# Optimization experiments

Hardware: AMD Instinct MI355X
Metric: run time of the kernel (lower is better)

## Reference

```python
import jax, jax.numpy as jnp
import numpy as np

U, IS, IT, D, DEG, L = 50000, 25000, 25000, 128, 16, 3


def _bipartite(key, n_users, n_items, deg):
    # symmetric normalized bipartite adjacency in COO, nnz = 2*n_users*deg
    ki = jax.random.fold_in(key, 1)
    u = jnp.repeat(jnp.arange(n_users, dtype=jnp.int32), deg)
    it = jax.random.randint(ki, (n_users * deg,), 0, n_items, dtype=jnp.int32)
    rows = jnp.concatenate([u, n_users + it])
    cols = jnp.concatenate([n_users + it, u])
    vals = jnp.full(rows.shape, 1.0 / deg, dtype=jnp.float32)
    return rows, cols, vals


def setup_inputs() -> dict:
    key = jax.random.key(0)
    ks = jax.random.split(key, 16)
    sc = 0.1
    inp = {
        'emb_s_user': jax.random.normal(ks[0], (U, D), jnp.float32) * sc,
        'emb_s_item': jax.random.normal(ks[1], (IS, D), jnp.float32) * sc,
        'emb_t_user': jax.random.normal(ks[2], (U, D), jnp.float32) * sc,
        'emb_t_item': jax.random.normal(ks[3], (IT, D), jnp.float32) * sc,
        'emb_share_user': jax.random.normal(ks[4], (U, D), jnp.float32) * sc,
    }
    inp['s_rows'], inp['s_cols'], inp['s_vals'] = _bipartite(ks[5], U, IS, DEG)
    inp['t_rows'], inp['t_cols'], inp['t_vals'] = _bipartite(ks[6], U, IT, DEG)
    inp['c_rows'], inp['c_cols'], inp['c_vals'] = _bipartite(ks[7], U, IS + IT, 2 * DEG)
    def lin(k, fi, fo):
        b = float(np.sqrt(6.0 / (fi + fo)))
        return jax.random.uniform(k, (fi, fo), jnp.float32, -b, b)
    inp.update({
        'Wd1': lin(ks[8], D, D), 'bd1': jnp.zeros((D,), jnp.float32),
        'Wd2': lin(ks[9], D, 2 * D), 'bd2': jnp.zeros((2 * D,), jnp.float32),
        'Wa1_s': lin(ks[10], 3 * D, D), 'ba1_s': jnp.zeros((D,), jnp.float32),
        'Wa2_s': lin(ks[11], D, 3), 'ba2_s': jnp.zeros((3,), jnp.float32),
        'Wa1_t': lin(ks[12], 3 * D, D), 'ba1_t': jnp.zeros((D,), jnp.float32),
        'Wa2_t': lin(ks[13], D, 3), 'ba2_t': jnp.zeros((3,), jnp.float32),
    })
    return inp


def _spmm(rows, cols, vals, x, n):
    # y = A @ x, A sparse COO (n x n)
    return jax.ops.segment_sum(vals[:, None] * x[cols], rows, num_segments=n)


def _lightgcn(rows, cols, vals, emb, n):
    acc, h = emb, emb
    for _ in range(L):  # layer-accumulating SpMM (mean of layer outputs)
        h = _spmm(rows, cols, vals, h, n)
        acc = acc + h
    return acc / (L + 1)


def _fuse(spe, intm, pop, W1, b1, W2, b2):
    x = jnp.concatenate([spe, intm, pop], axis=1)          # [B, 3D]
    h = jax.nn.relu(x @ W1 + b1)                           # [B, D]
    w = jax.nn.softmax(h @ W2 + b2, axis=1)                # [B, 3]
    return spe * w[:, 0:1] + intm * w[:, 1:2] + pop * w[:, 2:3]


def reference(emb_s_user, emb_s_item, emb_t_user, emb_t_item, emb_share_user,
              s_rows, s_cols, s_vals, t_rows, t_cols, t_vals,
              c_rows, c_cols, c_vals,
              Wd1, bd1, Wd2, bd2,
              Wa1_s, ba1_s, Wa2_s, ba2_s, Wa1_t, ba1_t, Wa2_t, ba2_t):
    # LightGCN propagation over the three graphs (get_G_emb)
    es = _lightgcn(s_rows, s_cols, s_vals, jnp.concatenate([emb_s_user, emb_s_item], 0), U + IS)
    et = _lightgcn(t_rows, t_cols, t_vals, jnp.concatenate([emb_t_user, emb_t_item], 0), U + IT)
    ec = _lightgcn(c_rows, c_cols, c_vals,
                   jnp.concatenate([emb_share_user, emb_s_item, emb_t_item], 0), U + IS + IT)
    user_s, user_t, user_sha = es[:U], et[:U], ec[:U]
    # disen_encoder (dropout inactive in eval): int / pop split
    h = jax.nn.relu(user_sha @ Wd1 + bd1)
    ip = h @ Wd2 + bd2
    int_u, pop_u = ip[:, :D], ip[:, D:]
    fused_s = _fuse(user_s, int_u, pop_u, Wa1_s, ba1_s, Wa2_s, ba2_s)
    fused_t = _fuse(user_t, int_u, pop_u, Wa1_t, ba1_t, Wa2_t, ba2_t)
    return jnp.concatenate([fused_s, fused_t], axis=0)  # [2U, D]
```

## Files before the change

### kernel.cpp

```cpp
#include <hip/hip_runtime.h>
#include <math.h>

#define UN 50000
#define DD 128
#define NUTILE 3125

typedef __attribute__((ext_vector_type(4))) float f32x4;
typedef __attribute__((ext_vector_type(8))) short s16x8;
typedef __attribute__((ext_vector_type(8))) unsigned short u16x8;
typedef __attribute__((ext_vector_type(4))) _Float16 f16x4;
typedef __attribute__((ext_vector_type(8))) _Float16 f16x8;
typedef unsigned short ushort_t;

__device__ __forceinline__ f32x4 mfma16(s16x8 a, s16x8 b, f32x4 c) {
  return __builtin_amdgcn_mfma_f32_16x16x32_bf16(a, b, c, 0, 0, 0);
}

__device__ __forceinline__ void split8(const float* x, s16x8& hi, s16x8& lo) {
  #pragma unroll
  for (int i = 0; i < 8; ++i) {
    float xv = x[i];
    unsigned xb = __float_as_uint(xv);
    unsigned h16 = (xb + 0x7fffu + ((xb >> 16) & 1u)) >> 16;
    float hf = __uint_as_float(h16 << 16);
    float lf = xv - hf;
    unsigned lb = __float_as_uint(lf);
    unsigned l16 = (lb + 0x7fffu + ((lb >> 16) & 1u)) >> 16;
    hi[i] = (short)h16;
    lo[i] = (short)l16;
  }
}

__global__ void zero_ints_k(int* p, int n) {
  int i = blockIdx.x * 256 + threadIdx.x;
  if (i < n) p[i] = 0;
}

__global__ void count_items_k(const int* __restrict__ cols, int E2, int* __restrict__ counts) {
  int base = (blockIdx.x * 256 + threadIdx.x) * 4;
  if (base + 3 < E2) {
    int4 c = *(const int4*)(cols + base);
    atomicAdd(&counts[c.x - UN], 1);
    atomicAdd(&counts[c.y - UN], 1);
    atomicAdd(&counts[c.z - UN], 1);
    atomicAdd(&counts[c.w - UN], 1);
  } else {
    for (int k = 0; k < 4; ++k)
      if (base + k < E2) atomicAdd(&counts[cols[base + k] - UN], 1);
  }
}

__global__ void scanA_k(const int* __restrict__ counts, int n, int* __restrict__ bsum) {
  __shared__ int sd[256];
  int t = threadIdx.x;
  int base = blockIdx.x * 1024 + t * 4;
  int s = 0;
  if (base + 3 < n) {
    int4 v = *(const int4*)(counts + base);
    s = v.x + v.y + v.z + v.w;
  } else {
    for (int k = 0; k < 4; ++k) if (base + k < n) s += counts[base + k];
  }
  sd[t] = s;
  __syncthreads();
  for (int off = 128; off > 0; off >>= 1) {
    if (t < off) sd[t] += sd[t + off];
    __syncthreads();
  }
  if (t == 0) bsum[blockIdx.x] = sd[0];
}

__global__ void scanB_k(int* __restrict__ bsum, int G) {
  __shared__ int sd[64];
  int t = threadIdx.x;
  sd[t] = (t < G) ? bsum[t] : 0;
  __syncthreads();
  int acc = 0;
  for (int i = 0; i < t; ++i) acc += sd[i];
  if (t < G) bsum[t] = acc;
}

__global__ void scanC_k(int* __restrict__ counts, int* __restrict__ offsets, int n,
                        const int* __restrict__ bsum) {
  __shared__ int sd[256];
  int t = threadIdx.x;
  int base = blockIdx.x * 1024 + t * 4;
  int c[4];
  int s = 0;
  #pragma unroll
  for (int k = 0; k < 4; ++k) {
    int idx = base + k;
    c[k] = (idx < n) ? counts[idx] : 0;
    s += c[k];
  }
  sd[t] = s;
  __syncthreads();
  for (int off = 1; off < 256; off <<= 1) {
    int v = (t >= off) ? sd[t - off] : 0;
    __syncthreads();
    sd[t] += v;
    __syncthreads();
  }
  int run = bsum[blockIdx.x] + ((t == 0) ? 0 : sd[t - 1]);
  #pragma unroll
  for (int k = 0; k < 4; ++k) {
    int idx = base + k;
    if (idx < n) { offsets[idx] = run; run += c[k]; counts[idx] = 0; }
  }
  if (base <= n - 1 && n - 1 < base + 4) offsets[n] = run;
}

__global__ void fill_lists_k(const int* __restrict__ cols, int E2,
                             const int* __restrict__ offsets, int* __restrict__ cursor,
                             int* __restrict__ lists, int shift) {
  int base = (blockIdx.x * 256 + threadIdx.x) * 4;
  if (base + 3 < E2) {
    int4 c = *(const int4*)(cols + base);
    int it0 = c.x - UN, it1 = c.y - UN, it2 = c.z - UN, it3 = c.w - UN;
    lists[offsets[it0] + atomicAdd(&cursor[it0], 1)] = base >> shift;
    lists[offsets[it1] + atomicAdd(&cursor[it1], 1)] = (base + 1) >> shift;
    lists[offsets[it2] + atomicAdd(&cursor[it2], 1)] = (base + 2) >> shift;
    lists[offsets[it3] + atomicAdd(&cursor[it3], 1)] = (base + 3) >> shift;
  } else {
    for (int k = 0; k < 4; ++k) {
      if (base + k < E2) {
        int it = cols[base + k] - UN;
        lists[offsets[it] + atomicAdd(&cursor[it], 1)] = (base + k) >> shift;
      }
    }
  }
}

__global__ void conv16_k(const float* __restrict__ in, _Float16* __restrict__ out) {
  int i = blockIdx.x * 256 + threadIdx.x;
  f32x4 v = ((const f32x4*)in)[i];
  f16x4 o;
  o[0] = (_Float16)v[0]; o[1] = (_Float16)v[1]; o[2] = (_Float16)v[2]; o[3] = (_Float16)v[3];
  ((f16x4*)out)[i] = o;
}

__global__ void initconv_k(const float* __restrict__ emb, float* __restrict__ acc,
                           _Float16* __restrict__ ue) {
  int i = blockIdx.x * 256 + threadIdx.x;
  f32x4 v = ((const f32x4*)emb)[i];
  ((f32x4*)acc)[i] = v * 0.25f;
  f16x4 o;
  o[0] = (_Float16)v[0]; o[1] = (_Float16)v[1]; o[2] = (_Float16)v[2]; o[3] = (_Float16)v[3];
  ((f16x4*)ue)[i] = o;
}

template<int DEG, bool WRITE_U, bool HAS_ITEM>
__global__ void hop_k(const int* __restrict__ cols, const int* __restrict__ ioff,
                      const int* __restrict__ ilst, const float* __restrict__ vals,
                      const _Float16* __restrict__ isrc, const _Float16* __restrict__ usrc,
                      _Float16* __restrict__ uout, _Float16* __restrict__ iout,
                      float* __restrict__ acc, int nitems) {
  int wid = (blockIdx.x * blockDim.x + threadIdx.x) >> 6;
  int lane = threadIdx.x & 63;
  int q = lane >> 4, cl = lane & 15;
  float v = vals[0];
  float s[8] = {};
  if (wid < UN) {
    int ebase = wid * DEG;
    #pragma unroll
    for (int p = 0; p < DEG / 4; ++p) {
      int item = cols[ebase + 4 * p + q] - UN;
      f16x8 x = *(const f16x8*)(isrc + (size_t)item * DD + cl * 8);
      #pragma unroll
      for (int r = 0; r < 8; ++r) s[r] += (float)x[r];
    }
    #pragma unroll
    for (int r = 0; r < 8; ++r) {
      s[r] += __shfl_xor(s[r], 16, 64);
      s[r] += __shfl_xor(s[r], 32, 64);
      s[r] *= v;
    }
    if (lane < 16) {
      if (WRITE_U) {
        f16x8 o;
        #pragma unroll
        for (int r = 0; r < 8; ++r) o[r] = (_Float16)s[r];
        *(f16x8*)(uout + (size_t)wid * DD + cl * 8) = o;
      }
      float* ap = acc + (size_t)wid * DD + cl * 8;
      f32x4 a0 = *(f32x4*)ap;
      f32x4 a1 = *(f32x4*)(ap + 4);
      #pragma unroll
      for (int r = 0; r < 4; ++r) { a0[r] += 0.25f * s[r]; a1[r] += 0.25f * s[r + 4]; }
      *(f32x4*)ap = a0;
      *(f32x4*)(ap + 4) = a1;
    }
  } else if (HAS_ITEM) {
    int it = wid - UN;
    if (it >= nitems) return;
    int b = ioff[it], e = ioff[it + 1];
    for (int j = b + q; j < e; j += 4) {
      int u = ilst[j];
      f16x8 x = *(const f16x8*)(usrc + (size_t)u * DD + cl * 8);
      #pragma unroll
      for (int r = 0; r < 8; ++r) s[r] += (float)x[r];
    }
    #pragma unroll
    for (int r = 0; r < 8; ++r) {
      s[r] += __shfl_xor(s[r], 16, 64);
      s[r] += __shfl_xor(s[r], 32, 64);
    }
    if (lane < 16) {
      f16x8 o;
      #pragma unroll
      for (int r = 0; r < 8; ++r) o[r] = (_Float16)(v * s[r]);
      *(f16x8*)(iout + (size_t)it * DD + cl * 8) = o;
    }
  }
}

__global__ void wprep_k(const float* __restrict__ W, ushort_t* __restrict__ whi,
                        ushort_t* __restrict__ wlo, int K, int N) {
  int idx = blockIdx.x * 256 + threadIdx.x;
  if (idx >= K * N) return;
  int i = idx & 7, l = (idx >> 3) & 63, tt = idx >> 9;
  int NT = N >> 4;
  int t = tt % NT, c = tt / NT;
  int k = c * 32 + 8 * (l >> 4) + i;
  int n = t * 16 + (l & 15);
  float xv = W[k * N + n];
  unsigned xb = __float_as_uint(xv);
  unsigned h16 = (xb + 0x7fffu + ((xb >> 16) & 1u)) >> 16;
  float hf = __uint_as_float(h16 << 16);
  float lf = xv - hf;
  unsigned lb = __float_as_uint(lf);
  unsigned l16 = (lb + 0x7fffu + ((lb >> 16) & 1u)) >> 16;
  whi[idx] = (ushort_t)h16;
  wlo[idx] = (ushort_t)l16;
}

template<int NCH, int NT, bool RELU, bool OUT16>
__global__ __launch_bounds__(256) void gemm_mfma_k(const float* __restrict__ X,
    const ushort_t* __restrict__ whi, const ushort_t* __restrict__ wlo,
    const float* __restrict__ bias, void* __restrict__ Ov) {
  __shared__ ushort_t sh[NT * 512];
  __shared__ ushort_t sl[NT * 512];
  int tid = threadIdx.x, lane = tid & 63;
  int utile = blockIdx.x * 4 + (tid >> 6);
  bool act = utile < NUTILE;
  const float* xrow = X + (size_t)(utile * 16 + (lane & 15)) * (NCH * 32);
  f32x4 acc[NT] = {};
  for (int c = 0; c < NCH; ++c) {
    __syncthreads();
    for (int q = tid; q < NT * 64; q += 256) {
      ((u16x8*)sh)[q] = ((const u16x8*)(whi + c * NT * 512))[q];
      ((u16x8*)sl)[q] = ((const u16x8*)(wlo + c * NT * 512))[q];
    }
    __syncthreads();
    if (!act) continue;
    int k0 = c * 32 + 8 * (lane >> 4);
    f32x4 xa = *(const f32x4*)(xrow + k0);
    f32x4 xb = *(const f32x4*)(xrow + k0 + 4);
    float xs8[8] = {xa[0], xa[1], xa[2], xa[3], xb[0], xb[1], xb[2], xb[3]};
    s16x8 ahi, alo;
    split8(xs8, ahi, alo);
    #pragma unroll
    for (int t = 0; t < NT; ++t) {
      s16x8 bh = ((const s16x8*)sh)[t * 64 + lane];
      s16x8 bl = ((const s16x8*)sl)[t * 64 + lane];
      acc[t] = mfma16(ahi, bh, acc[t]);
      acc[t] = mfma16(alo, bh, acc[t]);
      acc[t] = mfma16(ahi, bl, acc[t]);
    }
  }
  if (!act) return;
  int g4 = 4 * (lane >> 4);
  #pragma unroll
  for (int t = 0; t < NT; ++t) {
    int col = t * 16 + (lane & 15);
    float bb = bias[col];
    #pragma unroll
    for (int r = 0; r < 4; ++r) {
      float vv = acc[t][r] + bb;
      if (RELU) vv = fmaxf(vv, 0.f);
      size_t oidx = (size_t)(utile * 16 + g4 + r) * (NT * 16) + col;
      if (OUT16) ((_Float16*)Ov)[oidx] = (_Float16)vv;
      else ((float*)Ov)[oidx] = vv;
    }
  }
}

__global__ __launch_bounds__(256) void fuse_mfma_k(
    const float* __restrict__ spe, const _Float16* __restrict__ ip,
    const ushort_t* __restrict__ whi, const ushort_t* __restrict__ wlo,
    const float* __restrict__ b1, const float* __restrict__ W2,
    const float* __restrict__ b2, float* __restrict__ outp) {
  __shared__ ushort_t sh[8 * 512];
  __shared__ ushort_t sl[8 * 512];
  int tid = threadIdx.x, lane = tid & 63;
  int utile = blockIdx.x * 4 + (tid >> 6);
  bool act = utile < NUTILE;
  int rowA = utile * 16 + (lane & 15);
  f32x4 acc[8] = {};
  for (int c = 0; c < 12; ++c) {
    __syncthreads();
    for (int q = tid; q < 512; q += 256) {
      ((u16x8*)sh)[q] = ((const u16x8*)(whi + c * 4096))[q];
      ((u16x8*)sl)[q] = ((const u16x8*)(wlo + c * 4096))[q];
    }
    __syncthreads();
    if (!act) continue;
    int k0 = c * 32 + 8 * (lane >> 4);
    float xs8[8];
    if (k0 < 128) {
      f32x4 xa = *(const f32x4*)(spe + (size_t)rowA * 128 + k0);
      f32x4 xb = *(const f32x4*)(spe + (size_t)rowA * 128 + k0 + 4);
      xs8[0] = xa[0]; xs8[1] = xa[1]; xs8[2] = xa[2]; xs8[3] = xa[3];
      xs8[4] = xb[0]; xs8[5] = xb[1]; xs8[6] = xb[2]; xs8[7] = xb[3];
    } else {
      f16x8 xh = *(const f16x8*)(ip + (size_t)rowA * 256 + (k0 - 128));
      #pragma unroll
      for (int r = 0; r < 8; ++r) xs8[r] = (float)xh[r];
    }
    s16x8 ahi, alo;
    split8(xs8, ahi, alo);
    #pragma unroll
    for (int t = 0; t < 8; ++t) {
      s16x8 bh = ((const s16x8*)sh)[t * 64 + lane];
      s16x8 bl = ((const s16x8*)sl)[t * 64 + lane];
      acc[t] = mfma16(ahi, bh, acc[t]);
      acc[t] = mfma16(alo, bh, acc[t]);
      acc[t] = mfma16(ahi, bl, acc[t]);
    }
  }
  if (!act) return;
  float lg0[4] = {}, lg1[4] = {}, lg2[4] = {};
  #pragma unroll
  for (int t = 0; t < 8; ++t) {
    int col = t * 16 + (lane & 15);
    float bb = b1[col];
    float w20 = W2[col * 3 + 0], w21 = W2[col * 3 + 1], w22 = W2[col * 3 + 2];
    #pragma unroll
    for (int r = 0; r < 4; ++r) {
      float hv = fmaxf(acc[t][r] + bb, 0.f);
      lg0[r] += hv * w20; lg1[r] += hv * w21; lg2[r] += hv * w22;
    }
  }
  #pragma unroll
  for (int off = 1; off < 16; off <<= 1) {
    #pragma unroll
    for (int r = 0; r < 4; ++r) {
      lg0[r] += __shfl_xor(lg0[r], off, 64);
      lg1[r] += __shfl_xor(lg1[r], off, 64);
      lg2[r] += __shfl_xor(lg2[r], off, 64);
    }
  }
  float b20 = b2[0], b21 = b2[1], b22 = b2[2];
  int g4 = 4 * (lane >> 4);
  #pragma unroll
  for (int r = 0; r < 4; ++r) {
    float l0 = lg0[r] + b20, l1 = lg1[r] + b21, l2 = lg2[r] + b22;
    float m = fmaxf(l0, fmaxf(l1, l2));
    float e0 = expf(l0 - m), e1 = expf(l1 - m), e2 = expf(l2 - m);
    float inv = 1.f / (e0 + e1 + e2);
    float w0 = e0 * inv, w1 = e1 * inv, w2 = e2 * inv;
    size_t row = (size_t)(utile * 16 + g4 + r);
    #pragma unroll
    for (int t = 0; t < 8; ++t) {
      int col = t * 16 + (lane & 15);
      float sp = spe[row * 128 + col];
      float iu = (float)ip[row * 256 + col];
      float pu = (float)ip[row * 256 + 128 + col];
      outp[row * 128 + col] = sp * w0 + iu * w1 + pu * w2;
    }
  }
}

extern "C" void kernel_launch(void* const* d_in, const int* in_sizes, int n_in,
                              void* d_out, int out_size, void* d_ws, size_t ws_size,
                              hipStream_t stream) {
  const float* emb_s_user = (const float*)d_in[0];
  const float* emb_s_item = (const float*)d_in[1];
  const float* emb_t_user = (const float*)d_in[2];
  const float* emb_t_item = (const float*)d_in[3];
  const float* emb_sh_user = (const float*)d_in[4];
  const int* s_cols = (const int*)d_in[6];
  const float* s_vals = (const float*)d_in[7];
  const int* t_cols = (const int*)d_in[9];
  const float* t_vals = (const float*)d_in[10];
  const int* c_cols = (const int*)d_in[12];
  const float* c_vals = (const float*)d_in[13];
  const float* Wd1 = (const float*)d_in[14];
  const float* bd1 = (const float*)d_in[15];
  const float* Wd2 = (const float*)d_in[16];
  const float* bd2 = (const float*)d_in[17];
  const float* Wa1_s = (const float*)d_in[18];
  const float* ba1_s = (const float*)d_in[19];
  const float* Wa2_s = (const float*)d_in[20];
  const float* ba2_s = (const float*)d_in[21];
  const float* Wa1_t = (const float*)d_in[22];
  const float* ba1_t = (const float*)d_in[23];
  const float* Wa2_t = (const float*)d_in[24];
  const float* ba2_t = (const float*)d_in[25];

  char* wsb = (char*)d_ws;
  float* acc = (float*)wsb;
  _Float16* ip16 = (_Float16*)(wsb + 25600000);
  _Float16* u1 = (_Float16*)(wsb + 51200000);
  _Float16* i1 = (_Float16*)(wsb + 64000000);
  float* H = (float*)(wsb + 51200000);
  _Float16* i2 = (_Float16*)(wsb + 76800000);
  _Float16* ue = i2;
  _Float16* ie = (_Float16*)(wsb + 89600000);
  ushort_t* wbase = (ushort_t*)(wsb + 102400000);
  ushort_t* wd1h = wbase;
  ushort_t* wd1l = wbase + 16384;
  ushort_t* wd2h = wbase + 32768;
  ushort_t* wd2l = wbase + 65536;
  ushort_t* wa1sh = wbase + 98304;
  ushort_t* wa1sl = wbase + 147456;
  ushort_t* wa1th = wbase + 196608;
  ushort_t* wa1tl = wbase + 245760;
  int* ioff = (int*)(wsb + 103040000);
  int* icnt = (int*)(wsb + 103260032);
  int* bsum = (int*)(wsb + 103460096);
  int* ilst = (int*)(wsb + 103460608);

  float* outp = (float*)d_out;

  wprep_k<<<64, 256, 0, stream>>>(Wd1, wd1h, wd1l, 128, 128);
  wprep_k<<<128, 256, 0, stream>>>(Wd2, wd2h, wd2l, 128, 256);
  wprep_k<<<192, 256, 0, stream>>>(Wa1_s, wa1sh, wa1sl, 384, 128);
  wprep_k<<<192, 256, 0, stream>>>(Wa1_t, wa1th, wa1tl, 384, 128);
  conv16_k<<<3125, 256, 0, stream>>>(emb_s_item, ie);
  conv16_k<<<3125, 256, 0, stream>>>(emb_t_item, ie + (size_t)25000 * DD);

  auto run_graph = [&](const int* cols, const float* vals, int deg, int shift, int nitems,
                       const float* embU, const _Float16* isrc) {
    int E2 = UN * deg;
    int gE4 = (E2 + 1023) / 1024;
    int G = (nitems + 1023) / 1024;
    zero_ints_k<<<(nitems + 255) / 256, 256, 0, stream>>>(icnt, nitems);
    count_items_k<<<gE4, 256, 0, stream>>>(cols, E2, icnt);
    scanA_k<<<G, 256, 0, stream>>>(icnt, nitems, bsum);
    scanB_k<<<1, 64, 0, stream>>>(bsum, G);
    scanC_k<<<G, 256, 0, stream>>>(icnt, ioff, nitems, bsum);
    fill_lists_k<<<gE4, 256, 0, stream>>>(cols, E2, ioff, icnt, ilst, shift);
    initconv_k<<<6250, 256, 0, stream>>>(embU, acc, ue);
    int gH = (UN + nitems) / 4;
    int gU = UN / 4;
    if (deg == 32) {
      hop_k<32, true, true><<<gH, 256, 0, stream>>>(cols, ioff, ilst, vals, isrc, ue, u1, i1, acc, nitems);
      hop_k<32, false, true><<<gH, 256, 0, stream>>>(cols, ioff, ilst, vals, i1, u1, nullptr, i2, acc, nitems);
      hop_k<32, false, false><<<gU, 256, 0, stream>>>(cols, ioff, ilst, vals, i2, nullptr, nullptr, nullptr, acc, nitems);
    } else {
      hop_k<16, true, true><<<gH, 256, 0, stream>>>(cols, ioff, ilst, vals, isrc, ue, u1, i1, acc, nitems);
      hop_k<16, false, true><<<gH, 256, 0, stream>>>(cols, ioff, ilst, vals, i1, u1, nullptr, i2, acc, nitems);
      hop_k<16, false, false><<<gU, 256, 0, stream>>>(cols, ioff, ilst, vals, i2, nullptr, nullptr, nullptr, acc, nitems);
    }
  };

  run_graph(c_cols, c_vals, 32, 5, 50000, emb_sh_user, ie);
  gemm_mfma_k<4, 8, true, false><<<782, 256, 0, stream>>>(acc, wd1h, wd1l, bd1, H);
  gemm_mfma_k<4, 16, false, true><<<782, 256, 0, stream>>>(H, wd2h, wd2l, bd2, ip16);
  run_graph(s_cols, s_vals, 16, 4, 25000, emb_s_user, ie);
  fuse_mfma_k<<<782, 256, 0, stream>>>(acc, ip16, wa1sh, wa1sl, ba1_s, Wa2_s, ba2_s, outp);
  run_graph(t_cols, t_vals, 16, 4, 25000, emb_t_user, ie + (size_t)25000 * DD);
  fuse_mfma_k<<<782, 256, 0, stream>>>(acc, ip16, wa1th, wa1tl, ba1_t, Wa2_t, ba2_t, outp + (size_t)UN * DD);

  (void)in_sizes; (void)n_in; (void)out_size; (void)ws_size;
}
```

Measured before the change: 1.211 ms.

## Batch CSR build across graphs, drop fp32 accumulator, store fp16 hop outputs

The transpose-list construction for all three graphs now runs once, batched through combined count, scan and fill kernels, and the item lists are stored as 16-bit indices. The per-hop read-modify-write of an fp32 accumulator is removed. Each hop instead writes its fp16 user output, and the final hop averages the embedding and the three layer outputs into one fp16 result. The GEMM and fuse kernels read that result as fp16. Weight prep is merged into a single launch and index loads use nontemporal hints. This cuts launch count and memory traffic, at the cost of extra fp16 rounding of the accumulated embeddings.

```diff
diff --git a/kernel.cpp b/kernel.cpp
--- a/kernel.cpp
+++ b/kernel.cpp
@@ -31,22 +31,41 @@
   }
 }
 
-__global__ void zero_ints_k(int* p, int n) {
+__global__ void zero_k(int* p, int n) {
   int i = blockIdx.x * 256 + threadIdx.x;
   if (i < n) p[i] = 0;
 }
 
-__global__ void count_items_k(const int* __restrict__ cols, int E2, int* __restrict__ counts) {
-  int base = (blockIdx.x * 256 + threadIdx.x) * 4;
-  if (base + 3 < E2) {
-    int4 c = *(const int4*)(cols + base);
-    atomicAdd(&counts[c.x - UN], 1);
-    atomicAdd(&counts[c.y - UN], 1);
-    atomicAdd(&counts[c.z - UN], 1);
-    atomicAdd(&counts[c.w - UN], 1);
+__global__ void conv16_k(const float* __restrict__ in, _Float16* __restrict__ out) {
+  int i = blockIdx.x * 256 + threadIdx.x;
+  f32x4 v = ((const f32x4*)in)[i];
+  f16x4 o;
+  o[0] = (_Float16)v[0]; o[1] = (_Float16)v[1]; o[2] = (_Float16)v[2]; o[3] = (_Float16)v[3];
+  ((f16x4*)out)[i] = o;
+}
+
+#define CBLK 1563
+#define SBLK 782
+#define EC 1600000
+#define ES 800000
+
+__global__ void count_all_k(const int* __restrict__ cc, const int* __restrict__ sc,
+                            const int* __restrict__ tc, int* __restrict__ counts) {
+  int b = blockIdx.x, t = threadIdx.x;
+  const int* cols; int E, base, b0;
+  if (b < CBLK) { cols = cc; E = EC; base = 0; b0 = 0; }
+  else if (b < CBLK + SBLK) { cols = sc; E = ES; base = 50000; b0 = CBLK; }
+  else { cols = tc; E = ES; base = 75000; b0 = CBLK + SBLK; }
+  int e = (b - b0) * 1024 + t * 4;
+  if (e + 3 < E) {
+    int4 c4 = *(const int4*)(cols + e);
+    atomicAdd(&counts[base + c4.x - UN], 1);
+    atomicAdd(&counts[base + c4.y - UN], 1);
+    atomicAdd(&counts[base + c4.z - UN], 1);
+    atomicAdd(&counts[base + c4.w - UN], 1);
   } else {
     for (int k = 0; k < 4; ++k)
-      if (base + k < E2) atomicAdd(&counts[cols[base + k] - UN], 1);
+      if (e + k < E) atomicAdd(&counts[base + cols[e + k] - UN], 1);
   }
 }
 
@@ -71,13 +90,13 @@
 }
 
 __global__ void scanB_k(int* __restrict__ bsum, int G) {
-  __shared__ int sd[64];
+  __shared__ int sd[128];
   int t = threadIdx.x;
   sd[t] = (t < G) ? bsum[t] : 0;
   __syncthreads();
-  int acc = 0;
-  for (int i = 0; i < t; ++i) acc += sd[i];
-  if (t < G) bsum[t] = acc;
+  int a = 0;
+  for (int i = 0; i < t; ++i) a += sd[i];
+  if (t < G) bsum[t] = a;
 }
 
 __global__ void scanC_k(int* __restrict__ counts, int* __restrict__ offsets, int n,
@@ -110,51 +129,40 @@
   if (base <= n - 1 && n - 1 < base + 4) offsets[n] = run;
 }
 
-__global__ void fill_lists_k(const int* __restrict__ cols, int E2,
-                             const int* __restrict__ offsets, int* __restrict__ cursor,
-                             int* __restrict__ lists, int shift) {
-  int base = (blockIdx.x * 256 + threadIdx.x) * 4;
-  if (base + 3 < E2) {
-    int4 c = *(const int4*)(cols + base);
-    int it0 = c.x - UN, it1 = c.y - UN, it2 = c.z - UN, it3 = c.w - UN;
-    lists[offsets[it0] + atomicAdd(&cursor[it0], 1)] = base >> shift;
-    lists[offsets[it1] + atomicAdd(&cursor[it1], 1)] = (base + 1) >> shift;
-    lists[offsets[it2] + atomicAdd(&cursor[it2], 1)] = (base + 2) >> shift;
-    lists[offsets[it3] + atomicAdd(&cursor[it3], 1)] = (base + 3) >> shift;
+__global__ void fill_all_k(const int* __restrict__ cc, const int* __restrict__ sc,
+                           const int* __restrict__ tc, const int* __restrict__ offsets,
+                           int* __restrict__ cursor, ushort_t* __restrict__ lists) {
+  int b = blockIdx.x, t = threadIdx.x;
+  const int* cols; int E, base, b0, shift;
+  if (b < CBLK) { cols = cc; E = EC; base = 0; b0 = 0; shift = 5; }
+  else if (b < CBLK + SBLK) { cols = sc; E = ES; base = 50000; b0 = CBLK; shift = 4; }
+  else { cols = tc; E = ES; base = 75000; b0 = CBLK + SBLK; shift = 4; }
+  int e = (b - b0) * 1024 + t * 4;
+  if (e + 3 < E) {
+    int4 c4 = *(const int4*)(cols + e);
+    int b0i = base + c4.x - UN, b1i = base + c4.y - UN, b2i = base + c4.z - UN, b3i = base + c4.w - UN;
+    lists[offsets[b0i] + atomicAdd(&cursor[b0i], 1)] = (ushort_t)(e >> shift);
+    lists[offsets[b1i] + atomicAdd(&cursor[b1i], 1)] = (ushort_t)((e + 1) >> shift);
+    lists[offsets[b2i] + atomicAdd(&cursor[b2i], 1)] = (ushort_t)((e + 2) >> shift);
+    lists[offsets[b3i] + atomicAdd(&cursor[b3i], 1)] = (ushort_t)((e + 3) >> shift);
   } else {
     for (int k = 0; k < 4; ++k) {
-      if (base + k < E2) {
-        int it = cols[base + k] - UN;
-        lists[offsets[it] + atomicAdd(&cursor[it], 1)] = (base + k) >> shift;
+      if (e + k < E) {
+        int bi = base + cols[e + k] - UN;
+        lists[offsets[bi] + atomicAdd(&cursor[bi], 1)] = (ushort_t)((e + k) >> shift);
       }
     }
   }
 }
 
-__global__ void conv16_k(const float* __restrict__ in, _Float16* __restrict__ out) {
-  int i = blockIdx.x * 256 + threadIdx.x;
-  f32x4 v = ((const f32x4*)in)[i];
-  f16x4 o;
-  o[0] = (_Float16)v[0]; o[1] = (_Float16)v[1]; o[2] = (_Float16)v[2]; o[3] = (_Float16)v[3];
-  ((f16x4*)out)[i] = o;
-}
-
-__global__ void initconv_k(const float* __restrict__ emb, float* __restrict__ acc,
-                           _Float16* __restrict__ ue) {
-  int i = blockIdx.x * 256 + threadIdx.x;
-  f32x4 v = ((const f32x4*)emb)[i];
-  ((f32x4*)acc)[i] = v * 0.25f;
-  f16x4 o;
-  o[0] = (_Float16)v[0]; o[1] = (_Float16)v[1]; o[2] = (_Float16)v[2]; o[3] = (_Float16)v[3];
-  ((f16x4*)ue)[i] = o;
-}
-
-template<int DEG, bool WRITE_U, bool HAS_ITEM>
-__global__ void hop_k(const int* __restrict__ cols, const int* __restrict__ ioff,
-                      const int* __restrict__ ilst, const float* __restrict__ vals,
-                      const _Float16* __restrict__ isrc, const _Float16* __restrict__ usrc,
-                      _Float16* __restrict__ uout, _Float16* __restrict__ iout,
-                      float* __restrict__ acc, int nitems) {
+template<int DEG, int PH>
+__global__ __launch_bounds__(256) void hop_k(
+    const int* __restrict__ cols, const int* __restrict__ ioffg,
+    const ushort_t* __restrict__ ilst, const float* __restrict__ vals,
+    const _Float16* __restrict__ gu, const _Float16* __restrict__ gi,
+    const _Float16* __restrict__ ue, const _Float16* __restrict__ u1,
+    const _Float16* __restrict__ u2,
+    _Float16* __restrict__ uout, _Float16* __restrict__ iout, int nitems) {
   int wid = (blockIdx.x * blockDim.x + threadIdx.x) >> 6;
   int lane = threadIdx.x & 63;
   int q = lane >> 4, cl = lane & 15;
@@ -164,8 +172,8 @@
     int ebase = wid * DEG;
     #pragma unroll
     for (int p = 0; p < DEG / 4; ++p) {
-      int item = cols[ebase + 4 * p + q] - UN;
-      f16x8 x = *(const f16x8*)(isrc + (size_t)item * DD + cl * 8);
+      int item = __builtin_nontemporal_load(&cols[ebase + 4 * p + q]) - UN;
+      f16x8 x = *(const f16x8*)(gu + (size_t)item * DD + cl * 8);
       #pragma unroll
       for (int r = 0; r < 8; ++r) s[r] += (float)x[r];
     }
@@ -176,27 +184,30 @@
       s[r] *= v;
     }
     if (lane < 16) {
-      if (WRITE_U) {
+      size_t ro = (size_t)wid * DD + cl * 8;
+      if (PH == 3) {
+        f16x8 a = *(const f16x8*)(ue + ro);
+        f16x8 b = *(const f16x8*)(u1 + ro);
+        f16x8 c2 = *(const f16x8*)(u2 + ro);
+        f16x8 o;
+        #pragma unroll
+        for (int r = 0; r < 8; ++r)
+          o[r] = (_Float16)(0.25f * ((float)a[r] + (float)b[r] + (float)c2[r] + s[r]));
+        *(f16x8*)(uout + ro) = o;
+      } else {
         f16x8 o;
         #pragma unroll
         for (int r = 0; r < 8; ++r) o[r] = (_Float16)s[r];
-        *(f16x8*)(uout + (size_t)wid * DD + cl * 8) = o;
+        *(f16x8*)(uout + ro) = o;
       }
-      float* ap = acc + (size_t)wid * DD + cl * 8;
-      f32x4 a0 = *(f32x4*)ap;
-      f32x4 a1 = *(f32x4*)(ap + 4);
-      #pragma unroll
-      for (int r = 0; r < 4; ++r) { a0[r] += 0.25f * s[r]; a1[r] += 0.25f * s[r + 4]; }
-      *(f32x4*)ap = a0;
-      *(f32x4*)(ap + 4) = a1;
-    }
-  } else if (HAS_ITEM) {
+    }
+  } else if (PH != 3) {
     int it = wid - UN;
     if (it >= nitems) return;
-    int b = ioff[it], e = ioff[it + 1];
+    int b = ioffg[it], e = ioffg[it + 1];
     for (int j = b + q; j < e; j += 4) {
-      int u = ilst[j];
-      f16x8 x = *(const f16x8*)(usrc + (size_t)u * DD + cl * 8);
+      int u = (int)__builtin_nontemporal_load(&ilst[j]);
+      f16x8 x = *(const f16x8*)(gi + (size_t)u * DD + cl * 8);
       #pragma unroll
       for (int r = 0; r < 8; ++r) s[r] += (float)x[r];
     }
@@ -214,10 +225,18 @@
   }
 }
 
-__global__ void wprep_k(const float* __restrict__ W, ushort_t* __restrict__ whi,
-                        ushort_t* __restrict__ wlo, int K, int N) {
-  int idx = blockIdx.x * 256 + threadIdx.x;
-  if (idx >= K * N) return;
+__global__ void wprep_all_k(const float* __restrict__ Wd1, const float* __restrict__ Wd2,
+                            const float* __restrict__ Wa1s, const float* __restrict__ Wa1t,
+                            ushort_t* __restrict__ wd1h, ushort_t* __restrict__ wd1l,
+                            ushort_t* __restrict__ wd2h, ushort_t* __restrict__ wd2l,
+                            ushort_t* __restrict__ wash, ushort_t* __restrict__ wasl,
+                            ushort_t* __restrict__ wath, ushort_t* __restrict__ watl) {
+  int b = blockIdx.x, tid = threadIdx.x;
+  const float* W; ushort_t *wh, *wl; int N, idx;
+  if (b < 64)       { W = Wd1;  wh = wd1h; wl = wd1l; N = 128; idx = b * 256 + tid; }
+  else if (b < 192) { W = Wd2;  wh = wd2h; wl = wd2l; N = 256; idx = (b - 64) * 256 + tid; }
+  else if (b < 384) { W = Wa1s; wh = wash; wl = wasl; N = 128; idx = (b - 192) * 256 + tid; }
+  else              { W = Wa1t; wh = wath; wl = watl; N = 128; idx = (b - 384) * 256 + tid; }
   int i = idx & 7, l = (idx >> 3) & 63, tt = idx >> 9;
   int NT = N >> 4;
   int t = tt % NT, c = tt / NT;
@@ -230,12 +249,12 @@
   float lf = xv - hf;
   unsigned lb = __float_as_uint(lf);
   unsigned l16 = (lb + 0x7fffu + ((lb >> 16) & 1u)) >> 16;
-  whi[idx] = (ushort_t)h16;
-  wlo[idx] = (ushort_t)l16;
-}
-
-template<int NCH, int NT, bool RELU, bool OUT16>
-__global__ __launch_bounds__(256) void gemm_mfma_k(const float* __restrict__ X,
+  wh[idx] = (ushort_t)h16;
+  wl[idx] = (ushort_t)l16;
+}
+
+template<int NCH, int NT, bool RELU, bool OUT16, bool XF16>
+__global__ __launch_bounds__(256) void gemm_mfma_k(const void* __restrict__ Xv,
     const ushort_t* __restrict__ whi, const ushort_t* __restrict__ wlo,
     const float* __restrict__ bias, void* __restrict__ Ov) {
   __shared__ ushort_t sh[NT * 512];
@@ -243,7 +262,7 @@
   int tid = threadIdx.x, lane = tid & 63;
   int utile = blockIdx.x * 4 + (tid >> 6);
   bool act = utile < NUTILE;
-  const float* xrow = X + (size_t)(utile * 16 + (lane & 15)) * (NCH * 32);
+  size_t rowA = (size_t)(utile * 16 + (lane & 15)) * (NCH * 32);
   f32x4 acc[NT] = {};
   for (int c = 0; c < NCH; ++c) {
     __syncthreads();
@@ -254,9 +273,17 @@
     __syncthreads();
     if (!act) continue;
     int k0 = c * 32 + 8 * (lane >> 4);
-    f32x4 xa = *(const f32x4*)(xrow + k0);
-    f32x4 xb = *(const f32x4*)(xrow + k0 + 4);
-    float xs8[8] = {xa[0], xa[1], xa[2], xa[3], xb[0], xb[1], xb[2], xb[3]};
+    float xs8[8];
+    if (XF16) {
+      f16x8 xh = *(const f16x8*)((const _Float16*)Xv + rowA + k0);
+      #pragma unroll
+      for (int r = 0; r < 8; ++r) xs8[r] = (float)xh[r];
+    } else {
+      f32x4 xa = *(const f32x4*)((const float*)Xv + rowA + k0);
+      f32x4 xb = *(const f32x4*)((const float*)Xv + rowA + k0 + 4);
+      xs8[0] = xa[0]; xs8[1] = xa[1]; xs8[2] = xa[2]; xs8[3] = xa[3];
+      xs8[4] = xb[0]; xs8[5] = xb[1]; xs8[6] = xb[2]; xs8[7] = xb[3];
+    }
     s16x8 ahi, alo;
     split8(xs8, ahi, alo);
     #pragma unroll
@@ -286,7 +313,7 @@
 }
 
 __global__ __launch_bounds__(256) void fuse_mfma_k(
-    const float* __restrict__ spe, const _Float16* __restrict__ ip,
+    const _Float16* __restrict__ spe, const _Float16* __restrict__ ip,
     const ushort_t* __restrict__ whi, const ushort_t* __restrict__ wlo,
     const float* __restrict__ b1, const float* __restrict__ W2,
     const float* __restrict__ b2, float* __restrict__ outp) {
@@ -306,17 +333,12 @@
     __syncthreads();
     if (!act) continue;
     int k0 = c * 32 + 8 * (lane >> 4);
+    f16x8 xh;
+    if (k0 < 128) xh = *(const f16x8*)(spe + (size_t)rowA * 128 + k0);
+    else xh = *(const f16x8*)(ip + (size_t)rowA * 256 + (k0 - 128));
     float xs8[8];
-    if (k0 < 128) {
-      f32x4 xa = *(const f32x4*)(spe + (size_t)rowA * 128 + k0);
-      f32x4 xb = *(const f32x4*)(spe + (size_t)rowA * 128 + k0 + 4);
-      xs8[0] = xa[0]; xs8[1] = xa[1]; xs8[2] = xa[2]; xs8[3] = xa[3];
-      xs8[4] = xb[0]; xs8[5] = xb[1]; xs8[6] = xb[2]; xs8[7] = xb[3];
-    } else {
-      f16x8 xh = *(const f16x8*)(ip + (size_t)rowA * 256 + (k0 - 128));
-      #pragma unroll
-      for (int r = 0; r < 8; ++r) xs8[r] = (float)xh[r];
-    }
+    #pragma unroll
+    for (int r = 0; r < 8; ++r) xs8[r] = (float)xh[r];
     s16x8 ahi, alo;
     split8(xs8, ahi, alo);
     #pragma unroll
@@ -363,7 +385,7 @@
     #pragma unroll
     for (int t = 0; t < 8; ++t) {
       int col = t * 16 + (lane & 15);
-      float sp = spe[row * 128 + col];
+      float sp = (float)spe[row * 128 + col];
       float iu = (float)ip[row * 256 + col];
       float pu = (float)ip[row * 256 + 128 + col];
       outp[row * 128 + col] = sp * w0 + iu * w1 + pu * w2;
@@ -399,69 +421,71 @@
   const float* ba2_t = (const float*)d_in[25];
 
   char* wsb = (char*)d_ws;
-  float* acc = (float*)wsb;
-  _Float16* ip16 = (_Float16*)(wsb + 25600000);
-  _Float16* u1 = (_Float16*)(wsb + 51200000);
-  _Float16* i1 = (_Float16*)(wsb + 64000000);
-  float* H = (float*)(wsb + 51200000);
-  _Float16* i2 = (_Float16*)(wsb + 76800000);
-  _Float16* ue = i2;
-  _Float16* ie = (_Float16*)(wsb + 89600000);
-  ushort_t* wbase = (ushort_t*)(wsb + 102400000);
-  ushort_t* wd1h = wbase;
-  ushort_t* wd1l = wbase + 16384;
-  ushort_t* wd2h = wbase + 32768;
-  ushort_t* wd2l = wbase + 65536;
-  ushort_t* wa1sh = wbase + 98304;
-  ushort_t* wa1sl = wbase + 147456;
-  ushort_t* wa1th = wbase + 196608;
-  ushort_t* wa1tl = wbase + 245760;
-  int* ioff = (int*)(wsb + 103040000);
-  int* icnt = (int*)(wsb + 103260032);
-  int* bsum = (int*)(wsb + 103460096);
-  int* ilst = (int*)(wsb + 103460608);
+  _Float16* ue   = (_Float16*)(wsb);
+  _Float16* ie   = (_Float16*)(wsb + 12800000);
+  _Float16* u1b  = (_Float16*)(wsb + 25600000);
+  _Float16* u2b  = (_Float16*)(wsb + 38400000);
+  _Float16* i1b  = (_Float16*)(wsb + 51200000);
+  _Float16* i2b  = (_Float16*)(wsb + 64000000);
+  _Float16* spe  = (_Float16*)(wsb + 76800000);
+  _Float16* ip16 = (_Float16*)(wsb + 89600000);
+  float* H       = (float*)(wsb + 25600000);
+  ushort_t* wts  = (ushort_t*)(wsb + 115200000);
+  ushort_t* wd1h = wts;
+  ushort_t* wd1l = wts + 16384;
+  ushort_t* wd2h = wts + 32768;
+  ushort_t* wd2l = wts + 65536;
+  ushort_t* wash = wts + 98304;
+  ushort_t* wasl = wts + 147456;
+  ushort_t* wath = wts + 196608;
+  ushort_t* watl = wts + 245760;
+  int* counts = (int*)(wsb + 115789824);
+  int* ioff   = (int*)(wsb + 116189824);
+  int* bsum   = (int*)(wsb + 116589840);
+  ushort_t* ilst = (ushort_t*)(wsb + 116590240);
 
   float* outp = (float*)d_out;
 
-  wprep_k<<<64, 256, 0, stream>>>(Wd1, wd1h, wd1l, 128, 128);
-  wprep_k<<<128, 256, 0, stream>>>(Wd2, wd2h, wd2l, 128, 256);
-  wprep_k<<<192, 256, 0, stream>>>(Wa1_s, wa1sh, wa1sl, 384, 128);
-  wprep_k<<<192, 256, 0, stream>>>(Wa1_t, wa1th, wa1tl, 384, 128);
+  wprep_all_k<<<576, 256, 0, stream>>>(Wd1, Wd2, Wa1_s, Wa1_t,
+                                       wd1h, wd1l, wd2h, wd2l, wash, wasl, wath, watl);
   conv16_k<<<3125, 256, 0, stream>>>(emb_s_item, ie);
   conv16_k<<<3125, 256, 0, stream>>>(emb_t_item, ie + (size_t)25000 * DD);
-
-  auto run_graph = [&](const int* cols, const float* vals, int deg, int shift, int nitems,
-                       const float* embU, const _Float16* isrc) {
-    int E2 = UN * deg;
-    int gE4 = (E2 + 1023) / 1024;
-    int G = (nitems + 1023) / 1024;
-    zero_ints_k<<<(nitems + 255) / 256, 256, 0, stream>>>(icnt, nitems);
-    count_items_k<<<gE4, 256, 0, stream>>>(cols, E2, icnt);
-    scanA_k<<<G, 256, 0, stream>>>(icnt, nitems, bsum);
-    scanB_k<<<1, 64, 0, stream>>>(bsum, G);
-    scanC_k<<<G, 256, 0, stream>>>(icnt, ioff, nitems, bsum);
-    fill_lists_k<<<gE4, 256, 0, stream>>>(cols, E2, ioff, icnt, ilst, shift);
-    initconv_k<<<6250, 256, 0, stream>>>(embU, acc, ue);
-    int gH = (UN + nitems) / 4;
-    int gU = UN / 4;
-    if (deg == 32) {
-      hop_k<32, true, true><<<gH, 256, 0, stream>>>(cols, ioff, ilst, vals, isrc, ue, u1, i1, acc, nitems);
-      hop_k<32, false, true><<<gH, 256, 0, stream>>>(cols, ioff, ilst, vals, i1, u1, nullptr, i2, acc, nitems);
-      hop_k<32, false, false><<<gU, 256, 0, stream>>>(cols, ioff, ilst, vals, i2, nullptr, nullptr, nullptr, acc, nitems);
-    } else {
-      hop_k<16, true, true><<<gH, 256, 0, stream>>>(cols, ioff, ilst, vals, isrc, ue, u1, i1, acc, nitems);
-      hop_k<16, false, true><<<gH, 256, 0, stream>>>(cols, ioff, ilst, vals, i1, u1, nullptr, i2, acc, nitems);
-      hop_k<16, false, false><<<gU, 256, 0, stream>>>(cols, ioff, ilst, vals, i2, nullptr, nullptr, nullptr, acc, nitems);
-    }
-  };
-
-  run_graph(c_cols, c_vals, 32, 5, 50000, emb_sh_user, ie);
-  gemm_mfma_k<4, 8, true, false><<<782, 256, 0, stream>>>(acc, wd1h, wd1l, bd1, H);
-  gemm_mfma_k<4, 16, false, true><<<782, 256, 0, stream>>>(H, wd2h, wd2l, bd2, ip16);
-  run_graph(s_cols, s_vals, 16, 4, 25000, emb_s_user, ie);
-  fuse_mfma_k<<<782, 256, 0, stream>>>(acc, ip16, wa1sh, wa1sl, ba1_s, Wa2_s, ba2_s, outp);
-  run_graph(t_cols, t_vals, 16, 4, 25000, emb_t_user, ie + (size_t)25000 * DD);
-  fuse_mfma_k<<<782, 256, 0, stream>>>(acc, ip16, wa1th, wa1tl, ba1_t, Wa2_t, ba2_t, outp + (size_t)UN * DD);
+  zero_k<<<391, 256, 0, stream>>>(counts, 100000);
+  count_all_k<<<3127, 256, 0, stream>>>(c_cols, s_cols, t_cols, counts);
+  scanA_k<<<98, 256, 0, stream>>>(counts, 100000, bsum);
+  scanB_k<<<1, 128, 0, stream>>>(bsum, 98);
+  scanC_k<<<98, 256, 0, stream>>>(counts, ioff, 100000, bsum);
+  fill_all_k<<<3127, 256, 0, stream>>>(c_cols, s_cols, t_cols, ioff, counts, ilst);
+
+  conv16_k<<<6250, 256, 0, stream>>>(emb_sh_user, ue);
+  hop_k<32, 1><<<25000, 256, 0, stream>>>(c_cols, ioff, ilst, c_vals, ie, ue,
+                                          nullptr, nullptr, nullptr, u1b, i1b, 50000);
+  hop_k<32, 2><<<25000, 256, 0, stream>>>(c_cols, ioff, ilst, c_vals, i1b, u1b,
+                                          nullptr, nullptr, nullptr, u2b, i2b, 50000);
+  hop_k<32, 3><<<12500, 256, 0, stream>>>(c_cols, nullptr, nullptr, c_vals, i2b, nullptr,
+                                          ue, u1b, u2b, spe, nullptr, 0);
+  gemm_mfma_k<4, 8, true, false, true><<<782, 256, 0, stream>>>(spe, wd1h, wd1l, bd1, H);
+  gemm_mfma_k<4, 16, false, true, false><<<782, 256, 0, stream>>>(H, wd2h, wd2l, bd2, ip16);
+
+  conv16_k<<<6250, 256, 0, stream>>>(emb_s_user, ue);
+  hop_k<16, 1><<<18750, 256, 0, stream>>>(s_cols, ioff + 50000, ilst, s_vals, ie, ue,
+                                          nullptr, nullptr, nullptr, u1b, i1b, 25000);
+  hop_k<16, 2><<<18750, 256, 0, stream>>>(s_cols, ioff + 50000, ilst, s_vals, i1b, u1b,
+                                          nullptr, nullptr, nullptr, u2b, i2b, 25000);
+  hop_k<16, 3><<<12500, 256, 0, stream>>>(s_cols, nullptr, nullptr, s_vals, i2b, nullptr,
+                                          ue, u1b, u2b, spe, nullptr, 0);
+  fuse_mfma_k<<<782, 256, 0, stream>>>(spe, ip16, wash, wasl, ba1_s, Wa2_s, ba2_s, outp);
+
+  conv16_k<<<6250, 256, 0, stream>>>(emb_t_user, ue);
+  hop_k<16, 1><<<18750, 256, 0, stream>>>(t_cols, ioff + 75000, ilst, t_vals,
+                                          ie + (size_t)25000 * DD, ue,
+                                          nullptr, nullptr, nullptr, u1b, i1b, 25000);
+  hop_k<16, 2><<<18750, 256, 0, stream>>>(t_cols, ioff + 75000, ilst, t_vals, i1b, u1b,
+                                          nullptr, nullptr, nullptr, u2b, i2b, 25000);
+  hop_k<16, 3><<<12500, 256, 0, stream>>>(t_cols, nullptr, nullptr, t_vals, i2b, nullptr,
+                                          ue, u1b, u2b, spe, nullptr, 0);
+  fuse_mfma_k<<<782, 256, 0, stream>>>(spe, ip16, wath, watl, ba1_t, Wa2_t, ba2_t,
+                                       outp + (size_t)UN * DD);
 
   (void)in_sizes; (void)n_in; (void)out_size; (void)ws_size;
 }
```

New measurement: 1.168 ms. -3.6%, faster.
